# Optimization experiments

Hardware: AMD Instinct MI355X
Metric: run time of the kernel (lower is better)

## Reference

```python
import jax, jax.numpy as jnp
from jax import lax
import numpy as np

GROUPS = 32

def setup_inputs() -> dict:
    key = jax.random.key(0)
    ks = jax.random.split(key, 12)
    B, C, H, O, N = 4, 256, 256, 256, 4096
    s = 0.02  # small init scale to keep logits in a stable range
    x  = jax.random.normal(ks[0], (B, C, N), dtype=jnp.float32)
    Wk = jax.random.normal(ks[1], (H, C), dtype=jnp.float32) * s
    bk = jax.random.normal(ks[2], (H,), dtype=jnp.float32) * s
    Wq = jax.random.normal(ks[3], (H, C), dtype=jnp.float32) * s
    bq = jax.random.normal(ks[4], (H,), dtype=jnp.float32) * s
    W1 = jax.random.normal(ks[5], (H, C), dtype=jnp.float32) * s
    b1 = jax.random.normal(ks[6], (H,), dtype=jnp.float32) * s
    # grouped conv1d kernel: (out_ch, in_ch // groups, kw) in 'OIH' layout
    W2 = jax.random.normal(ks[7], (H, H // GROUPS, 3), dtype=jnp.float32) * s
    b2 = jax.random.normal(ks[8], (H,), dtype=jnp.float32) * s
    W3 = jax.random.normal(ks[9], (O, H), dtype=jnp.float32) * s
    b3 = jax.random.normal(ks[10], (O,), dtype=jnp.float32) * s
    return {"x": x, "Wk": Wk, "bk": bk, "Wq": Wq, "bq": bq,
            "W1": W1, "b1": b1, "W2": W2, "b2": b2, "W3": W3, "b3": b3}


def reference(x, Wk, bk, Wq, bq, W1, b1, W2, b2, W3, b3):
    # k: 1x1 conv then permute(0,2,1) -> [B, N, H]
    k = jnp.einsum('hc,bcn->bnh', Wk, x) + bk
    # q: 1x1 conv -> [B, H, N]
    q = jnp.einsum('hc,bcn->bhn', Wq, x) + bq[None, :, None]
    # sim = softmax(k @ q, dim=-2): softmax over the FIRST N axis (rows)
    sim = jax.nn.softmax(jnp.einsum('bnh,bhm->bnm', k, q), axis=-2)  # [B, N, N]
    # v path: 1x1 conv -> grouped 3-tap conv (pad=1) -> ReLU -> 1x1 conv
    v1 = jnp.einsum('hc,bcn->bhn', W1, x) + b1[None, :, None]
    v2 = lax.conv_general_dilated(
        v1, W2, window_strides=(1,), padding='SAME',
        feature_group_count=GROUPS,
        dimension_numbers=('NCH', 'OIH', 'NCH')) + b2[None, :, None]
    v2 = jax.nn.relu(v2)
    v = jnp.einsum('oh,bhn->bon', W3, v2) + b3[None, :, None]  # [B, O, N]
    # out = v @ sim -> [B, O, N]
    return jnp.einsum('bon,bnm->bom', v, sim)
```

## Files before the change

kernel.cpp:

```cpp
#include <hip/hip_runtime.h>


#define B_ 4
#define C_ 256
#define H_ 256
#define O_ 256
#define N_ 4096
#define NSPLIT 4
#define SPAN (N_ / NSPLIT)
#define ITERS (SPAN / 32)

typedef short short8 __attribute__((ext_vector_type(8)));
typedef float floatx4 __attribute__((ext_vector_type(4)));
typedef float floatx16 __attribute__((ext_vector_type(16)));

__device__ __forceinline__ unsigned short f2bf(float f) {
  unsigned u = __float_as_uint(f);
  u = (u + 0x7fffu + ((u >> 16) & 1u)) >> 16;
  return (unsigned short)u;
}
__device__ __forceinline__ float bf2f(unsigned short u) {
  return __uint_as_float(((unsigned)u) << 16);
}
__device__ __forceinline__ floatx4 mfma16(short8 a, short8 b, floatx4 c) {
  return __builtin_amdgcn_mfma_f32_16x16x32_bf16(a, b, c, 0, 0, 0);
}
__device__ __forceinline__ floatx16 mfma32(short8 a, short8 b, floatx16 c) {
  return __builtin_amdgcn_mfma_f32_32x32x16_bf16(a, b, c, 0, 0, 0);
}
__device__ __forceinline__ unsigned pack2bf(float a, float b) {
  return __builtin_amdgcn_perm(__float_as_uint(b) + 0x8000u,
                               __float_as_uint(a) + 0x8000u, 0x07060302u);
}

__global__ __launch_bounds__(256) void prep_kernel(
    const float* __restrict__ Wk, const float* __restrict__ Wq,
    const float* __restrict__ W1, const float* __restrict__ W3,
    unsigned short* __restrict__ wk, unsigned short* __restrict__ wq,
    unsigned short* __restrict__ w1, unsigned short* __restrict__ w3) {
  int i = blockIdx.x * 256 + threadIdx.x;
  wk[i] = f2bf(Wk[i]);
  wq[i] = f2bf(Wq[i]);
  w1[i] = f2bf(W1[i]);
  w3[i] = f2bf(W3[i]);
}

__global__ __launch_bounds__(256) void transpose_kernel(
    const float* __restrict__ x, unsigned short* __restrict__ xt) {
  __shared__ unsigned short tile[64][66];
  const int gid = blockIdx.x;
  const int b  = gid >> 8;
  const int ct = (gid >> 6) & 3;
  const int nt = gid & 63;
  const int c0 = ct * 64, n0 = nt * 64;
  const int t = threadIdx.x;
  const float* xb = x + ((size_t)b * C_ + c0) * N_ + n0;
#pragma unroll
  for (int rr = 0; rr < 4; ++rr) {
    const int c = (t >> 4) + rr * 16;
    const floatx4 v = *reinterpret_cast<const floatx4*>(
        xb + (size_t)c * N_ + (t & 15) * 4);
#pragma unroll
    for (int i = 0; i < 4; ++i) tile[c][(t & 15) * 4 + i] = f2bf(v[i]);
  }
  __syncthreads();
  unsigned short* xo = xt + ((size_t)b * N_ + n0) * C_ + c0;
#pragma unroll
  for (int rr = 0; rr < 2; ++rr) {
    const int nr = (t >> 3) + rr * 32;
    short8 pk;
#pragma unroll
    for (int i = 0; i < 8; ++i) pk[i] = (short)tile[(t & 7) * 8 + i][nr];
    *reinterpret_cast<short8*>(xo + (size_t)nr * C_ + (t & 7) * 8) = pk;
  }
}

__global__ __launch_bounds__(256) void gemm1_kernel(
    const unsigned short* __restrict__ xt,
    const unsigned short* __restrict__ wk, const unsigned short* __restrict__ wq,
    const unsigned short* __restrict__ w1,
    const float* __restrict__ bk, const float* __restrict__ bq,
    const float* __restrict__ b1,
    unsigned short* __restrict__ ko, unsigned short* __restrict__ qo,
    unsigned short* __restrict__ v1o) {
  const int lane = threadIdx.x & 63;
  const int wid  = blockIdx.x * 4 + (threadIdx.x >> 6);
  const int b  = wid >> 9;
  const int r  = wid & 511;
  const int hh = r >> 8;
  const int nt = r & 255;
  const int n0 = nt * 16;
  const int m  = lane & 15;
  const int q  = lane >> 4;

  const unsigned short* xrow = xt + ((size_t)(b * N_) + n0 + m) * C_;
  const unsigned short* Ws[3] = {wk, wq, w1};

  floatx4 acc[3][8];
  const floatx4 z = {0.f, 0.f, 0.f, 0.f};
#pragma unroll
  for (int o = 0; o < 3; ++o)
#pragma unroll
    for (int tt = 0; tt < 8; ++tt) acc[o][tt] = z;

  for (int cs = 0; cs < 8; ++cs) {
    const int cb = cs * 32 + q * 8;
    short8 af = *reinterpret_cast<const short8*>(xrow + cb);
#pragma unroll
    for (int o = 0; o < 3; ++o) {
#pragma unroll
      for (int tt = 0; tt < 8; ++tt) {
        const int h0 = (hh * 8 + tt) * 16;
        short8 bf = *reinterpret_cast<const short8*>(Ws[o] + (h0 + m) * C_ + cb);
        acc[o][tt] = mfma16(af, bf, acc[o][tt]);
      }
    }
  }

#pragma unroll
  for (int tt = 0; tt < 8; ++tt) {
    const int ks16 = hh * 8 + tt;
    const float bias = bk[ks16 * 16 + m];
#pragma unroll
    for (int r2 = 0; r2 < 4; ++r2) {
      const int n = n0 + q * 4 + r2;
      ko[((size_t)(b * 128 + (n >> 5))) * 8192 + ks16 * 512 + (n & 31) * 16 + m] =
          f2bf(acc[0][tt][r2] + bias);
    }
  }
  const float* biases[2] = {bq, b1};
  unsigned short* outs[2] = {qo, v1o};
#pragma unroll
  for (int o = 0; o < 2; ++o) {
#pragma unroll
    for (int tt = 0; tt < 8; ++tt) {
      const int h0 = (hh * 8 + tt) * 16;
      const float bias = biases[o][h0 + m];
#pragma unroll
      for (int r2 = 0; r2 < 4; ++r2) {
        const int n = n0 + q * 4 + r2;
        outs[o][(b * N_ + n) * H_ + h0 + m] = f2bf(acc[o + 1][tt][r2] + bias);
      }
    }
  }
}

__global__ __launch_bounds__(256) void convgemm2_kernel(
    const unsigned short* __restrict__ v1, const float* __restrict__ W2,
    const float* __restrict__ b2, const unsigned short* __restrict__ w3,
    const float* __restrict__ b3, unsigned short* __restrict__ vo) {
  __shared__ unsigned short v2L[32][264];

  const int h   = threadIdx.x;
  const int blk = blockIdx.x;
  const int b   = blk >> 7;
  const int nc  = blk & 127;
  const int n0  = nc * 32;
  const int g8  = h & ~7;

  {
    float w[24];
#pragma unroll
    for (int i = 0; i < 24; ++i) w[i] = W2[h * 24 + i];
    const float bias = b2[h];
    const unsigned short* vb = v1 + (size_t)b * (N_ * H_) + g8;

    float fp[8], fc[8], fn[8];
    if (n0 == 0) {
#pragma unroll
      for (int i = 0; i < 8; ++i) fp[i] = 0.f;
    } else {
      short8 u = *reinterpret_cast<const short8*>(vb + (size_t)(n0 - 1) * H_);
#pragma unroll
      for (int i = 0; i < 8; ++i) fp[i] = bf2f((unsigned short)u[i]);
    }
    {
      short8 u = *reinterpret_cast<const short8*>(vb + (size_t)n0 * H_);
#pragma unroll
      for (int i = 0; i < 8; ++i) fc[i] = bf2f((unsigned short)u[i]);
    }
#pragma unroll 1
    for (int ns = 0; ns < 32; ++ns) {
      const int n = n0 + ns;
      if (n + 1 < N_) {
        short8 u = *reinterpret_cast<const short8*>(vb + (size_t)(n + 1) * H_);
#pragma unroll
        for (int i = 0; i < 8; ++i) fn[i] = bf2f((unsigned short)u[i]);
      } else {
#pragma unroll
        for (int i = 0; i < 8; ++i) fn[i] = 0.f;
      }
      float a = bias;
#pragma unroll
      for (int i = 0; i < 8; ++i)
        a += w[i * 3] * fp[i] + w[i * 3 + 1] * fc[i] + w[i * 3 + 2] * fn[i];
      v2L[ns][h] = f2bf(fmaxf(a, 0.f));
#pragma unroll
      for (int i = 0; i < 8; ++i) { fp[i] = fc[i]; fc[i] = fn[i]; }
    }
  }
  __syncthreads();

  const int ln = threadIdx.x & 63;
  const int wv = threadIdx.x >> 6;
  const int m  = ln & 31;
  const int hl = ln >> 5;

  floatx16 acc2[2];
#pragma unroll
  for (int ot = 0; ot < 2; ++ot)
#pragma unroll
    for (int r = 0; r < 16; ++r) acc2[ot][r] = 0.f;

#pragma unroll
  for (int ks = 0; ks < 16; ++ks) {
    short8 bfr = *reinterpret_cast<const short8*>(&v2L[m][ks * 16 + hl * 8]);
#pragma unroll
    for (int ot = 0; ot < 2; ++ot) {
      const int o0 = wv * 64 + ot * 32;
      short8 afr = *reinterpret_cast<const short8*>(
          w3 + (o0 + m) * H_ + ks * 16 + hl * 8);
      acc2[ot] = mfma32(afr, bfr, acc2[ot]);
    }
  }

  const int kn  = (m >> 4) & 1;
  const int nlo = m & 15;
  unsigned short* vc = vo + ((size_t)(b * 128 + nc) * 2 + kn) * 4096 + nlo;
#pragma unroll
  for (int ot = 0; ot < 2; ++ot)
#pragma unroll
    for (int r = 0; r < 16; ++r) {
      const int o = wv * 64 + ot * 32 + (r & 3) + 8 * (r >> 2) + 4 * hl;
      vc[o * 16] = f2bf(acc2[ot][r] + b3[o]);
    }
}

__global__ __launch_bounds__(256, 2) void attn_kernel(
    const unsigned short* __restrict__ kbf, const unsigned short* __restrict__ qbf,
    const unsigned short* __restrict__ vbf,
    unsigned short* __restrict__ pacc, float* __restrict__ pml) {
  __shared__ __attribute__((aligned(16))) char smem[2][32768];

  const int ln  = threadIdx.x & 63;
  const int wv  = threadIdx.x >> 6;
  const int gid = blockIdx.x;
  const int b   = gid & 3;
  const int s   = (gid >> 2) & 3;
  const int mt128 = gid >> 4;
  const int mt32  = mt128 * 4 + wv;
  const int m0  = mt32 * 32;
  const int m   = ln & 31;
  const int hl  = ln >> 5;
  const int lane_base = m * 32 + hl * 16;
  const int hlsh = hl * 16;

  const unsigned short* qrow = qbf + ((size_t)b * N_ + m0 + m) * H_ + hl * 8;
  short8 qf[16];
#pragma unroll
  for (int ks = 0; ks < 16; ++ks)
    qf[ks] = *reinterpret_cast<const short8*>(qrow + ks * 16);

  floatx16 acc[8];
#pragma unroll
  for (int t = 0; t < 8; ++t)
#pragma unroll
    for (int r = 0; r < 16; ++r) acc[t][r] = 0.f;
  float Lp = 0.f;

  auto stage = [&](int bfi, int nc) {
    const size_t row = (size_t)(b * 128 + s * 32 + nc);
    const char* kg = (const char*)(kbf + row * 8192);
    const char* vg = (const char*)(vbf + row * 8192);
    char* lk = &smem[bfi][0];
    char* lv = &smem[bfi][16384];
#pragma unroll
    for (int j = 0; j < 4; ++j) {
      const int ofs = j * 4096 + wv * 1024 + ln * 16;
      __builtin_amdgcn_global_load_lds(
          (const __attribute__((address_space(1))) void*)(kg + ofs),
          (__attribute__((address_space(3))) void*)(lk + ofs), 16, 0, 0);
      __builtin_amdgcn_global_load_lds(
          (const __attribute__((address_space(1))) void*)(vg + ofs),
          (__attribute__((address_space(3))) void*)(lv + ofs), 16, 0, 0);
    }
  };

  stage(0, 0);
  int bufi = 0;

#pragma unroll 1
  for (int nc = 0; nc < ITERS; ++nc) {
    __syncthreads();
    if (nc + 1 < ITERS) stage(bufi ^ 1, nc + 1);

    const char* sk = &smem[bufi][0];
    const char* sv = &smem[bufi][16384];

    floatx16 sacc;
#pragma unroll
    for (int r = 0; r < 16; ++r) sacc[r] = 0.f;
#pragma unroll
    for (int ks = 0; ks < 16; ++ks) {
      short8 kf = *reinterpret_cast<const short8*>(sk + lane_base + ks * 1024);
      sacc = mfma32(kf, qf[ks], sacc);
    }

    unsigned wpk[8];
#pragma unroll
    for (int r4 = 0; r4 < 4; ++r4) {
      float a = __expf(sacc[r4]),     bb = __expf(sacc[r4 + 4]);
      float c = __expf(sacc[r4 + 8]), d  = __expf(sacc[r4 + 12]);
      Lp += (a + bb) + (c + d);
      wpk[r4]     = pack2bf(a, bb);
      wpk[r4 + 4] = pack2bf(c, d);
    }

    short8 pf0, pf1;
#pragma unroll
    for (int j = 0; j < 8; ++j) {
      const int srcLane = m + ((j >> 2) << 5);
      const int u0 = __shfl((int)wpk[j & 3],       srcLane);
      const int u1 = __shfl((int)wpk[(j & 3) + 4], srcLane);
      pf0[j] = (short)((unsigned)u0 >> hlsh);
      pf1[j] = (short)((unsigned)u1 >> hlsh);
    }

#pragma unroll
    for (int ot = 0; ot < 8; ++ot) {
      short8 vf0 = *reinterpret_cast<const short8*>(
          sv + lane_base + ot * 1024);
      short8 vf1 = *reinterpret_cast<const short8*>(
          sv + lane_base + 8192 + ot * 1024);
      acc[ot] = mfma32(vf0, pf0, acc[ot]);
      acc[ot] = mfma32(vf1, pf1, acc[ot]);
    }
    bufi ^= 1;
  }

  float Lv = Lp + __shfl_xor(Lp, 32);
  const float invL = 1.f / Lv;

  const int pwid = (b * 128 + mt32) * NSPLIT + s;
  unsigned short* pa = pacc + (size_t)pwid * (O_ * 32);
#pragma unroll
  for (int ot = 0; ot < 8; ++ot)
#pragma unroll
    for (int r = 0; r < 16; ++r) {
      const int o = ot * 32 + (r & 3) + 8 * (r >> 2) + 4 * hl;
      pa[o * 32 + m] = f2bf(acc[ot][r] * invL);
    }
  if (hl == 0) pml[pwid * 32 + m] = Lv;
}

__global__ __launch_bounds__(256) void combine_kernel(
    const unsigned short* __restrict__ pacc, const float* __restrict__ pml,
    float* __restrict__ out) {
  const int blk = blockIdx.x;
  const int b   = blk >> 7;
  const int mw  = blk & 127;
  const int o   = threadIdx.x;
  const int base = (b * 128 + mw) * NSPLIT;

  __shared__ float w[NSPLIT][32];
  if (threadIdx.x < 32) {
    const int c = threadIdx.x;
    float L[NSPLIT], sum = 0.f;
#pragma unroll
    for (int sp = 0; sp < NSPLIT; ++sp) {
      L[sp] = pml[(base + sp) * 32 + c];
      sum += L[sp];
    }
    const float inv = 1.f / sum;
#pragma unroll
    for (int sp = 0; sp < NSPLIT; ++sp) w[sp][c] = L[sp] * inv;
  }
  __syncthreads();

  float res[32];
#pragma unroll
  for (int c = 0; c < 32; ++c) res[c] = 0.f;
#pragma unroll
  for (int sp = 0; sp < NSPLIT; ++sp) {
    const unsigned short* pa =
        pacc + (size_t)(base + sp) * (O_ * 32) + o * 32;
#pragma unroll
    for (int c8 = 0; c8 < 4; ++c8) {
      short8 u = *reinterpret_cast<const short8*>(pa + c8 * 8);
#pragma unroll
      for (int i = 0; i < 8; ++i)
        res[c8 * 8 + i] =
            fmaf(w[sp][c8 * 8 + i], bf2f((unsigned short)u[i]), res[c8 * 8 + i]);
    }
  }
  float* ob = out + ((size_t)(b * O_ + o)) * N_ + mw * 32;
#pragma unroll
  for (int c4 = 0; c4 < 8; ++c4) {
    floatx4 v4 = {res[c4 * 4], res[c4 * 4 + 1], res[c4 * 4 + 2], res[c4 * 4 + 3]};
    *reinterpret_cast<floatx4*>(ob + c4 * 4) = v4;
  }
}

extern "C" void kernel_launch(void* const* d_in, const int* in_sizes, int n_in,
                              void* d_out, int out_size, void* d_ws, size_t ws_size,
                              hipStream_t stream) {
  const float* x  = (const float*)d_in[0];
  const float* Wk = (const float*)d_in[1];
  const float* bk = (const float*)d_in[2];
  const float* Wq = (const float*)d_in[3];
  const float* bq = (const float*)d_in[4];
  const float* W1 = (const float*)d_in[5];
  const float* b1 = (const float*)d_in[6];
  const float* W2 = (const float*)d_in[7];
  const float* b2 = (const float*)d_in[8];
  const float* W3 = (const float*)d_in[9];
  const float* b3 = (const float*)d_in[10];
  float* out = (float*)d_out;

  char* ws = (char*)d_ws;
  const size_t SZ = (size_t)B_ * N_ * H_ * sizeof(unsigned short);
  unsigned short* wkbf = (unsigned short*)(ws);
  unsigned short* wqbf = (unsigned short*)(ws + 131072);
  unsigned short* w1bf = (unsigned short*)(ws + 262144);
  unsigned short* w3bf = (unsigned short*)(ws + 393216);
  char* base = ws + 524288;
  unsigned short* kbf  = (unsigned short*)(base);
  unsigned short* qbf  = (unsigned short*)(base + SZ);
  unsigned short* vbf  = (unsigned short*)(base + 2 * SZ);
  unsigned short* xtbf = (unsigned short*)(base + 3 * SZ);
  unsigned short* v1bf = (unsigned short*)(base + 4 * SZ);
  unsigned short* pacc = (unsigned short*)(base + 3 * SZ);
  float*          pml  = (float*)(base + 7 * SZ);

  prep_kernel<<<256, 256, 0, stream>>>(Wk, Wq, W1, W3, wkbf, wqbf, w1bf, w3bf);
  transpose_kernel<<<1024, 256, 0, stream>>>(x, xtbf);
  gemm1_kernel<<<512, 256, 0, stream>>>(xtbf, wkbf, wqbf, w1bf, bk, bq, b1,
                                        kbf, qbf, v1bf);
  convgemm2_kernel<<<512, 256, 0, stream>>>(v1bf, W2, b2, w3bf, b3, vbf);
  attn_kernel<<<512, 256, 0, stream>>>(kbf, qbf, vbf, pacc, pml);
  combine_kernel<<<512, 256, 0, stream>>>(pacc, pml, out);
}
```

Measured before the change: 255.9 us.

## Fuse prep into transpose, fold combine into attention via counters, use permlane32 swap

Merges the weight-conversion kernel into the transpose launch as extra blocks. The split-N combine step moves into the attention kernel: the last of the four split blocks, detected with an atomic counter, does the reduction. Together these remove two kernel launches. When the builtin is available, the 16 shuffles used to rearrange softmax probabilities into MFMA B-operand layout are replaced by permlane32_swap, which cuts cross-lane traffic in the inner loop. The costs are threadfence and atomic overhead plus a serialized tail on the last block of each group.

```diff
diff --git a/kernel.cpp b/kernel.cpp
--- a/kernel.cpp
+++ b/kernel.cpp
@@ -13,6 +13,7 @@
 typedef short short8 __attribute__((ext_vector_type(8)));
 typedef float floatx4 __attribute__((ext_vector_type(4)));
 typedef float floatx16 __attribute__((ext_vector_type(16)));
+typedef unsigned uint2v __attribute__((ext_vector_type(2)));
 
 __device__ __forceinline__ unsigned short f2bf(float f) {
   unsigned u = __float_as_uint(f);
@@ -33,27 +34,29 @@
                                __float_as_uint(a) + 0x8000u, 0x07060302u);
 }
 
-__global__ __launch_bounds__(256) void prep_kernel(
+__global__ __launch_bounds__(256) void prep_transpose_kernel(
+    const float* __restrict__ x, unsigned short* __restrict__ xt,
     const float* __restrict__ Wk, const float* __restrict__ Wq,
     const float* __restrict__ W1, const float* __restrict__ W3,
     unsigned short* __restrict__ wk, unsigned short* __restrict__ wq,
-    unsigned short* __restrict__ w1, unsigned short* __restrict__ w3) {
-  int i = blockIdx.x * 256 + threadIdx.x;
-  wk[i] = f2bf(Wk[i]);
-  wq[i] = f2bf(Wq[i]);
-  w1[i] = f2bf(W1[i]);
-  w3[i] = f2bf(W3[i]);
-}
-
-__global__ __launch_bounds__(256) void transpose_kernel(
-    const float* __restrict__ x, unsigned short* __restrict__ xt) {
+    unsigned short* __restrict__ w1, unsigned short* __restrict__ w3,
+    unsigned int* __restrict__ cnt) {
   __shared__ unsigned short tile[64][66];
   const int gid = blockIdx.x;
+  const int t = threadIdx.x;
+  if (gid >= 1024) {
+    const int i = (gid - 1024) * 256 + t;
+    wk[i] = f2bf(Wk[i]);
+    wq[i] = f2bf(Wq[i]);
+    w1[i] = f2bf(W1[i]);
+    w3[i] = f2bf(W3[i]);
+    if (gid == 1024 && t < 128) cnt[t] = 0u;
+    return;
+  }
   const int b  = gid >> 8;
   const int ct = (gid >> 6) & 3;
   const int nt = gid & 63;
   const int c0 = ct * 64, n0 = nt * 64;
-  const int t = threadIdx.x;
   const float* xb = x + ((size_t)b * C_ + c0) * N_ + n0;
 #pragma unroll
   for (int rr = 0; rr < 4; ++rr) {
@@ -239,7 +242,8 @@
 __global__ __launch_bounds__(256, 2) void attn_kernel(
     const unsigned short* __restrict__ kbf, const unsigned short* __restrict__ qbf,
     const unsigned short* __restrict__ vbf,
-    unsigned short* __restrict__ pacc, float* __restrict__ pml) {
+    unsigned short* __restrict__ pacc, float* __restrict__ pml,
+    unsigned int* __restrict__ cnt, float* __restrict__ out) {
   __shared__ __attribute__((aligned(16))) char smem[2][32768];
 
   const int ln  = threadIdx.x & 63;
@@ -253,7 +257,6 @@
   const int m   = ln & 31;
   const int hl  = ln >> 5;
   const int lane_base = m * 32 + hl * 16;
-  const int hlsh = hl * 16;
 
   const unsigned short* qrow = qbf + ((size_t)b * N_ + m0 + m) * H_ + hl * 8;
   short8 qf[16];
@@ -306,17 +309,41 @@
       sacc = mfma32(kf, qf[ks], sacc);
     }
 
+    short8 pf0, pf1;
+#if __has_builtin(__builtin_amdgcn_permlane32_swap)
+    unsigned d[8];
+#pragma unroll
+    for (int i = 0; i < 8; ++i) {
+      const float a = __expf(sacc[2 * i]);
+      const float bb = __expf(sacc[2 * i + 1]);
+      Lp += a + bb;
+      d[i] = pack2bf(a, bb);
+    }
+#pragma unroll
+    for (int g = 0; g < 2; ++g) {
+      uint2v r0 = __builtin_amdgcn_permlane32_swap(d[4 * g + 0], d[4 * g + 2],
+                                                   false, false);
+      uint2v r1 = __builtin_amdgcn_permlane32_swap(d[4 * g + 1], d[4 * g + 3],
+                                                   false, false);
+      d[4 * g + 0] = r0.x; d[4 * g + 2] = r0.y;
+      d[4 * g + 1] = r1.x; d[4 * g + 3] = r1.y;
+    }
+    union { unsigned u[4]; short8 s8; } c0, c1;
+    c0.u[0] = d[0]; c0.u[1] = d[1]; c0.u[2] = d[2]; c0.u[3] = d[3];
+    c1.u[0] = d[4]; c1.u[1] = d[5]; c1.u[2] = d[6]; c1.u[3] = d[7];
+    pf0 = c0.s8;
+    pf1 = c1.s8;
+#else
+    float pv[16];
+#pragma unroll
+    for (int r = 0; r < 16; ++r) { pv[r] = __expf(sacc[r]); Lp += pv[r]; }
     unsigned wpk[8];
 #pragma unroll
     for (int r4 = 0; r4 < 4; ++r4) {
-      float a = __expf(sacc[r4]),     bb = __expf(sacc[r4 + 4]);
-      float c = __expf(sacc[r4 + 8]), d  = __expf(sacc[r4 + 12]);
-      Lp += (a + bb) + (c + d);
-      wpk[r4]     = pack2bf(a, bb);
-      wpk[r4 + 4] = pack2bf(c, d);
-    }
-
-    short8 pf0, pf1;
+      wpk[r4]     = pack2bf(pv[r4], pv[r4 + 4]);
+      wpk[r4 + 4] = pack2bf(pv[r4 + 8], pv[r4 + 12]);
+    }
+    const int hlsh = hl * 16;
 #pragma unroll
     for (int j = 0; j < 8; ++j) {
       const int srcLane = m + ((j >> 2) << 5);
@@ -325,11 +352,11 @@
       pf0[j] = (short)((unsigned)u0 >> hlsh);
       pf1[j] = (short)((unsigned)u1 >> hlsh);
     }
+#endif
 
 #pragma unroll
     for (int ot = 0; ot < 8; ++ot) {
-      short8 vf0 = *reinterpret_cast<const short8*>(
-          sv + lane_base + ot * 1024);
+      short8 vf0 = *reinterpret_cast<const short8*>(sv + lane_base + ot * 1024);
       short8 vf1 = *reinterpret_cast<const short8*>(
           sv + lane_base + 8192 + ot * 1024);
       acc[ot] = mfma32(vf0, pf0, acc[ot]);
@@ -351,53 +378,59 @@
       pa[o * 32 + m] = f2bf(acc[ot][r] * invL);
     }
   if (hl == 0) pml[pwid * 32 + m] = Lv;
-}
-
-__global__ __launch_bounds__(256) void combine_kernel(
-    const unsigned short* __restrict__ pacc, const float* __restrict__ pml,
-    float* __restrict__ out) {
-  const int blk = blockIdx.x;
-  const int b   = blk >> 7;
-  const int mw  = blk & 127;
-  const int o   = threadIdx.x;
-  const int base = (b * 128 + mw) * NSPLIT;
-
-  __shared__ float w[NSPLIT][32];
-  if (threadIdx.x < 32) {
-    const int c = threadIdx.x;
+
+  __syncthreads();
+  int* sflag = (int*)&smem[0][0];
+  float* wsm = (float*)&smem[0][64];
+  if (threadIdx.x == 0) {
+    __threadfence();
+    sflag[0] = (int)atomicAdd(&cnt[b * 32 + mt128], 1u);
+  }
+  __syncthreads();
+  if (sflag[0] != NSPLIT - 1) return;
+  __threadfence();
+
+  const int base4 = (b * 128 + mt32) * NSPLIT;
+  if (hl == 0) {
+    const int c = ln;
     float L[NSPLIT], sum = 0.f;
 #pragma unroll
     for (int sp = 0; sp < NSPLIT; ++sp) {
-      L[sp] = pml[(base + sp) * 32 + c];
+      L[sp] = pml[(base4 + sp) * 32 + c];
       sum += L[sp];
     }
     const float inv = 1.f / sum;
 #pragma unroll
-    for (int sp = 0; sp < NSPLIT; ++sp) w[sp][c] = L[sp] * inv;
-  }
-  __syncthreads();
-
-  float res[32];
-#pragma unroll
-  for (int c = 0; c < 32; ++c) res[c] = 0.f;
-#pragma unroll
-  for (int sp = 0; sp < NSPLIT; ++sp) {
-    const unsigned short* pa =
-        pacc + (size_t)(base + sp) * (O_ * 32) + o * 32;
-#pragma unroll
-    for (int c8 = 0; c8 < 4; ++c8) {
-      short8 u = *reinterpret_cast<const short8*>(pa + c8 * 8);
+    for (int sp = 0; sp < NSPLIT; ++sp)
+      wsm[wv * 128 + sp * 32 + c] = L[sp] * inv;
+  }
+  const int m8 = (ln & 3) * 8;
+  float wreg[NSPLIT][8];
+#pragma unroll
+  for (int sp = 0; sp < NSPLIT; ++sp)
+#pragma unroll
+    for (int i = 0; i < 8; ++i)
+      wreg[sp][i] = wsm[wv * 128 + sp * 32 + m8 + i];
+
+#pragma unroll 1
+  for (int ot = 0; ot < 16; ++ot) {
+    const int orow = ot * 16 + (ln >> 2);
+    float res[8];
+#pragma unroll
+    for (int i = 0; i < 8; ++i) res[i] = 0.f;
+#pragma unroll
+    for (int sp = 0; sp < NSPLIT; ++sp) {
+      short8 u = *reinterpret_cast<const short8*>(
+          pacc + (size_t)(base4 + sp) * (O_ * 32) + orow * 32 + m8);
 #pragma unroll
       for (int i = 0; i < 8; ++i)
-        res[c8 * 8 + i] =
-            fmaf(w[sp][c8 * 8 + i], bf2f((unsigned short)u[i]), res[c8 * 8 + i]);
-    }
-  }
-  float* ob = out + ((size_t)(b * O_ + o)) * N_ + mw * 32;
-#pragma unroll
-  for (int c4 = 0; c4 < 8; ++c4) {
-    floatx4 v4 = {res[c4 * 4], res[c4 * 4 + 1], res[c4 * 4 + 2], res[c4 * 4 + 3]};
-    *reinterpret_cast<floatx4*>(ob + c4 * 4) = v4;
+        res[i] = fmaf(wreg[sp][i], bf2f((unsigned short)u[i]), res[i]);
+    }
+    float* op = out + ((size_t)(b * O_) + orow) * N_ + mt32 * 32 + m8;
+    floatx4 v0 = {res[0], res[1], res[2], res[3]};
+    floatx4 v1 = {res[4], res[5], res[6], res[7]};
+    *reinterpret_cast<floatx4*>(op) = v0;
+    *reinterpret_cast<floatx4*>(op + 4) = v1;
   }
 }
 
@@ -431,12 +464,12 @@
   unsigned short* v1bf = (unsigned short*)(base + 4 * SZ);
   unsigned short* pacc = (unsigned short*)(base + 3 * SZ);
   float*          pml  = (float*)(base + 7 * SZ);
-
-  prep_kernel<<<256, 256, 0, stream>>>(Wk, Wq, W1, W3, wkbf, wqbf, w1bf, w3bf);
-  transpose_kernel<<<1024, 256, 0, stream>>>(x, xtbf);
+  unsigned int*   cnt  = (unsigned int*)(base + 7 * SZ + 262144);
+
+  prep_transpose_kernel<<<1280, 256, 0, stream>>>(
+      x, xtbf, Wk, Wq, W1, W3, wkbf, wqbf, w1bf, w3bf, cnt);
   gemm1_kernel<<<512, 256, 0, stream>>>(xtbf, wkbf, wqbf, w1bf, bk, bq, b1,
                                         kbf, qbf, v1bf);
   convgemm2_kernel<<<512, 256, 0, stream>>>(v1bf, W2, b2, w3bf, b3, vbf);
-  attn_kernel<<<512, 256, 0, stream>>>(kbf, qbf, vbf, pacc, pml);
-  combine_kernel<<<512, 256, 0, stream>>>(pacc, pml, out);
-}
+  attn_kernel<<<512, 256, 0, stream>>>(kbf, qbf, vbf, pacc, pml, cnt, out);
+}
```

Measured after the change: 278.2 us. +8.7%, slower.

## Swizzle K/V LDS layout, use permlane32_swap for P, merge prep kernels

Applied to the files above, without the earlier changes.

Three changes. First, the K and V tiles written by the producer kernels are XOR-swizzled, and the attention kernel reads them with a matching swizzled lane_base, aiming to cut LDS bank conflicts. Second, the 16 shuffles that turned the exp'd scores into the P operand are replaced by permlane32_swap exchanges when the builtin is available. Third, the weight-cast and transpose kernels are merged into one launch. These are coordinated layout edits across producers and consumer, so any index mismatch would silently corrupt the output.

```diff
diff --git a/kernel.cpp b/kernel.cpp
--- a/kernel.cpp
+++ b/kernel.cpp
@@ -13,6 +13,7 @@
 typedef short short8 __attribute__((ext_vector_type(8)));
 typedef float floatx4 __attribute__((ext_vector_type(4)));
 typedef float floatx16 __attribute__((ext_vector_type(16)));
+typedef unsigned uint2v __attribute__((ext_vector_type(2)));
 
 __device__ __forceinline__ unsigned short f2bf(float f) {
   unsigned u = __float_as_uint(f);
@@ -33,27 +34,27 @@
                                __float_as_uint(a) + 0x8000u, 0x07060302u);
 }
 
-__global__ __launch_bounds__(256) void prep_kernel(
+__global__ __launch_bounds__(256) void prep_transpose_kernel(
+    const float* __restrict__ x, unsigned short* __restrict__ xt,
     const float* __restrict__ Wk, const float* __restrict__ Wq,
     const float* __restrict__ W1, const float* __restrict__ W3,
     unsigned short* __restrict__ wk, unsigned short* __restrict__ wq,
     unsigned short* __restrict__ w1, unsigned short* __restrict__ w3) {
-  int i = blockIdx.x * 256 + threadIdx.x;
-  wk[i] = f2bf(Wk[i]);
-  wq[i] = f2bf(Wq[i]);
-  w1[i] = f2bf(W1[i]);
-  w3[i] = f2bf(W3[i]);
-}
-
-__global__ __launch_bounds__(256) void transpose_kernel(
-    const float* __restrict__ x, unsigned short* __restrict__ xt) {
   __shared__ unsigned short tile[64][66];
   const int gid = blockIdx.x;
+  const int t = threadIdx.x;
+  if (gid >= 1024) {
+    const int i = (gid - 1024) * 256 + t;
+    wk[i] = f2bf(Wk[i]);
+    wq[i] = f2bf(Wq[i]);
+    w1[i] = f2bf(W1[i]);
+    w3[i] = f2bf(W3[i]);
+    return;
+  }
   const int b  = gid >> 8;
   const int ct = (gid >> 6) & 3;
   const int nt = gid & 63;
   const int c0 = ct * 64, n0 = nt * 64;
-  const int t = threadIdx.x;
   const float* xb = x + ((size_t)b * C_ + c0) * N_ + n0;
 #pragma unroll
   for (int rr = 0; rr < 4; ++rr) {
@@ -117,6 +118,7 @@
     }
   }
 
+  const int msw = m ^ ((q & 1) << 3);
 #pragma unroll
   for (int tt = 0; tt < 8; ++tt) {
     const int ks16 = hh * 8 + tt;
@@ -124,7 +126,7 @@
 #pragma unroll
     for (int r2 = 0; r2 < 4; ++r2) {
       const int n = n0 + q * 4 + r2;
-      ko[((size_t)(b * 128 + (n >> 5))) * 8192 + ks16 * 512 + (n & 31) * 16 + m] =
+      ko[((size_t)(b * 128 + (n >> 5))) * 8192 + ks16 * 512 + (n & 31) * 16 + msw] =
           f2bf(acc[0][tt][r2] + bias);
     }
   }
@@ -225,14 +227,14 @@
   }
 
   const int kn  = (m >> 4) & 1;
-  const int nlo = m & 15;
-  unsigned short* vc = vo + ((size_t)(b * 128 + nc) * 2 + kn) * 4096 + nlo;
+  const int nsw = (m & 15) ^ (hl << 3);
+  unsigned short* vkn = vo + ((size_t)(b * 128 + nc) * 2 + kn) * 4096;
 #pragma unroll
   for (int ot = 0; ot < 2; ++ot)
 #pragma unroll
     for (int r = 0; r < 16; ++r) {
       const int o = wv * 64 + ot * 32 + (r & 3) + 8 * (r >> 2) + 4 * hl;
-      vc[o * 16] = f2bf(acc2[ot][r] + b3[o]);
+      vkn[o * 16 + nsw] = f2bf(acc2[ot][r] + b3[o]);
     }
 }
 
@@ -252,8 +254,7 @@
   const int m0  = mt32 * 32;
   const int m   = ln & 31;
   const int hl  = ln >> 5;
-  const int lane_base = m * 32 + hl * 16;
-  const int hlsh = hl * 16;
+  const int lane_base = m * 32 + (hl ^ ((m >> 2) & 1)) * 16;
 
   const unsigned short* qrow = qbf + ((size_t)b * N_ + m0 + m) * H_ + hl * 8;
   short8 qf[16];
@@ -306,17 +307,41 @@
       sacc = mfma32(kf, qf[ks], sacc);
     }
 
+    short8 pf0, pf1;
+#if __has_builtin(__builtin_amdgcn_permlane32_swap)
+    unsigned d[8];
+#pragma unroll
+    for (int i = 0; i < 8; ++i) {
+      const float a = __expf(sacc[2 * i]);
+      const float bb = __expf(sacc[2 * i + 1]);
+      Lp += a + bb;
+      d[i] = pack2bf(a, bb);
+    }
+#pragma unroll
+    for (int g = 0; g < 2; ++g) {
+      uint2v r0 = __builtin_amdgcn_permlane32_swap(d[4 * g + 0], d[4 * g + 2],
+                                                   false, false);
+      uint2v r1 = __builtin_amdgcn_permlane32_swap(d[4 * g + 1], d[4 * g + 3],
+                                                   false, false);
+      d[4 * g + 0] = r0.x; d[4 * g + 2] = r0.y;
+      d[4 * g + 1] = r1.x; d[4 * g + 3] = r1.y;
+    }
+    union { unsigned u[4]; short8 s8; } c0, c1;
+    c0.u[0] = d[0]; c0.u[1] = d[1]; c0.u[2] = d[2]; c0.u[3] = d[3];
+    c1.u[0] = d[4]; c1.u[1] = d[5]; c1.u[2] = d[6]; c1.u[3] = d[7];
+    pf0 = c0.s8;
+    pf1 = c1.s8;
+#else
+    float pv[16];
+#pragma unroll
+    for (int r = 0; r < 16; ++r) { pv[r] = __expf(sacc[r]); Lp += pv[r]; }
     unsigned wpk[8];
 #pragma unroll
     for (int r4 = 0; r4 < 4; ++r4) {
-      float a = __expf(sacc[r4]),     bb = __expf(sacc[r4 + 4]);
-      float c = __expf(sacc[r4 + 8]), d  = __expf(sacc[r4 + 12]);
-      Lp += (a + bb) + (c + d);
-      wpk[r4]     = pack2bf(a, bb);
-      wpk[r4 + 4] = pack2bf(c, d);
-    }
-
-    short8 pf0, pf1;
+      wpk[r4]     = pack2bf(pv[r4], pv[r4 + 4]);
+      wpk[r4 + 4] = pack2bf(pv[r4 + 8], pv[r4 + 12]);
+    }
+    const int hlsh = hl * 16;
 #pragma unroll
     for (int j = 0; j < 8; ++j) {
       const int srcLane = m + ((j >> 2) << 5);
@@ -325,11 +350,11 @@
       pf0[j] = (short)((unsigned)u0 >> hlsh);
       pf1[j] = (short)((unsigned)u1 >> hlsh);
     }
+#endif
 
 #pragma unroll
     for (int ot = 0; ot < 8; ++ot) {
-      short8 vf0 = *reinterpret_cast<const short8*>(
-          sv + lane_base + ot * 1024);
+      short8 vf0 = *reinterpret_cast<const short8*>(sv + lane_base + ot * 1024);
       short8 vf1 = *reinterpret_cast<const short8*>(
           sv + lane_base + 8192 + ot * 1024);
       acc[ot] = mfma32(vf0, pf0, acc[ot]);
@@ -432,8 +457,8 @@
   unsigned short* pacc = (unsigned short*)(base + 3 * SZ);
   float*          pml  = (float*)(base + 7 * SZ);
 
-  prep_kernel<<<256, 256, 0, stream>>>(Wk, Wq, W1, W3, wkbf, wqbf, w1bf, w3bf);
-  transpose_kernel<<<1024, 256, 0, stream>>>(x, xtbf);
+  prep_transpose_kernel<<<1280, 256, 0, stream>>>(
+      x, xtbf, Wk, Wq, W1, W3, wkbf, wqbf, w1bf, w3bf);
   gemm1_kernel<<<512, 256, 0, stream>>>(xtbf, wkbf, wqbf, w1bf, bk, bq, b1,
                                         kbf, qbf, v1bf);
   convgemm2_kernel<<<512, 256, 0, stream>>>(v1bf, W2, b2, w3bf, b3, vbf);
```

Result: faster. 248.1 us (-3.0%).
